# Optimization experiments

Hardware: AMD Instinct MI355X
Metric: run time of the kernel (lower is better)

Reference implementation:

```python
import jax, jax.numpy as jnp
import numpy as np

B, T, N, M, D = 4, 64, 32, 32, 128  # batch, time, price points, liquidity points, feature dim


def setup_inputs() -> dict:
    key = jax.random.key(0)
    ks = jax.random.split(key, 6)
    w = lambda k, shape: jax.random.normal(k, shape, jnp.float32) * 0.05
    return {
        "price": jax.random.normal(ks[0], (B, T, N, D), jnp.float32),
        "liquid": jax.random.normal(ks[1], (B, T, M, D), jnp.float32),
        "W_p": w(ks[2], (D, D)), "b_p": jnp.zeros((D,), jnp.float32),
        "W_v": w(ks[3], (D, D)), "b_v": jnp.zeros((D,), jnp.float32),
        "W1": w(ks[4], (4 * D, D)), "b1": jnp.zeros((D,), jnp.float32),
        "W2": w(ks[5], (D, D)), "b2": jnp.zeros((D,), jnp.float32),
    }


def reference(price, liquid, W_p, b_p, W_v, b_v, W1, b1, W2, b2):
    # proj_p / proj_v
    p = price @ W_p + b_p    # [B, T, N, D]
    v = liquid @ W_v + b_v   # [B, T, M, D]
    p4 = p[:, :, :, None, :]  # [B, T, N, 1, D]
    v4 = v[:, :, None, :, :]  # [B, T, 1, M, D]
    prod = p4 * v4            # [B, T, N, M, D]
    absdiff = jnp.abs(p4 - v4)
    full = (p.shape[0], p.shape[1], p.shape[2], v.shape[2], p.shape[3])
    pair = jnp.concatenate(
        [jnp.broadcast_to(p4, full), jnp.broadcast_to(v4, full), prod, absdiff],
        axis=-1,
    )  # [B, T, N, M, 4D]
    h = jax.nn.silu(pair @ W1 + b1)  # [B, T, N, M, D]
    grid = h @ W2 + b2               # [B, T, N, M, D]
    return grid.reshape(grid.shape[0], grid.shape[1], grid.shape[2] * grid.shape[3], grid.shape[4])
```

## Files before the change

kernel.cpp:

```cpp
#include <hip/hip_runtime.h>


typedef short  short8  __attribute__((ext_vector_type(8)));
typedef float  f32x4   __attribute__((ext_vector_type(4)));
typedef float  f32x16  __attribute__((ext_vector_type(16)));

#define DEV static __device__ __forceinline__

DEV float bf2f(unsigned short h) {
  unsigned u = ((unsigned)h) << 16;
  float f;
  __builtin_memcpy(&f, &u, 4);
  return f;
}
DEV unsigned short f2bf(float f) {
  unsigned u;
  __builtin_memcpy(&u, &f, 4);
  unsigned r = (u + 0x7FFFu + ((u >> 16) & 1u)) >> 16;
  return (unsigned short)r;
}

__global__ void k0_prep(const float* __restrict__ Wp, const float* __restrict__ bp,
                        const float* __restrict__ Wv, const float* __restrict__ bv,
                        const float* __restrict__ W1, const float* __restrict__ b1,
                        const float* __restrict__ W2,
                        unsigned short* __restrict__ w1cd, unsigned short* __restrict__ w2sw,
                        unsigned short* __restrict__ wpsw, unsigned short* __restrict__ gpsw,
                        unsigned short* __restrict__ wvsw, unsigned short* __restrict__ gvsw,
                        float* __restrict__ c1) {
  int t = blockIdx.x * 256 + threadIdx.x;
  if (t < 32768) {
    int j = t & 7, lane = (t >> 3) & 63, r2 = t >> 9;
    int ct = r2 & 3, kt = r2 >> 2;
    int k = kt * 16 + (lane >> 5) * 8 + j;
    int c = ct * 32 + (lane & 31);
    w1cd[t] = f2bf(W1[(256 + k) * 128 + c]);
  } else if (t < 114688) {
    int e = t - 32768;
    int sec = e >> 14;
    int f = e & 16383;
    int j = f & 7, lane = (f >> 3) & 63, r2 = f >> 9;
    if (sec == 0) {
      int ct = r2 & 3, kt = r2 >> 2;
      int k = kt * 16 + (lane >> 5) * 8 + j;
      int c = ct * 32 + (lane & 31);
      w2sw[f] = f2bf(W2[k * 128 + c]);
    } else {
      int kt = r2 & 3, ct = r2 >> 2;
      int k = kt * 32 + ((lane >> 4) & 3) * 8 + j;
      int n = ct * 16 + (lane & 15);
      if (sec == 1) {
        wpsw[f] = f2bf(Wp[k * 128 + n]);
      } else if (sec == 2) {
        float s = 0.f;
        for (int e2 = 0; e2 < 128; e2++) s += Wp[k * 128 + e2] * W1[e2 * 128 + n];
        gpsw[f] = f2bf(s);
      } else if (sec == 3) {
        wvsw[f] = f2bf(Wv[k * 128 + n]);
      } else {
        float s = 0.f;
        for (int e2 = 0; e2 < 128; e2++) s += Wv[k * 128 + e2] * W1[(128 + e2) * 128 + n];
        gvsw[f] = f2bf(s);
      }
    }
  } else if (t < 114816) {
    int c = t - 114688;
    float s = b1[c];
    for (int e2 = 0; e2 < 128; e2++)
      s += bp[e2] * W1[e2 * 128 + c] + bv[e2] * W1[(128 + e2) * 128 + c];
    c1[c] = s;
  }
}

__global__ __launch_bounds__(256, 2) void k1_proj(
    const float* __restrict__ price, const float* __restrict__ liquid,
    const float* __restrict__ bp, const float* __restrict__ bv, const float* __restrict__ c1,
    const unsigned short* __restrict__ wpsw, const unsigned short* __restrict__ gpsw,
    const unsigned short* __restrict__ wvsw, const unsigned short* __restrict__ gvsw,
    unsigned short* __restrict__ pbf, unsigned short* __restrict__ vbf,
    float* __restrict__ pAc, unsigned short* __restrict__ vbsw) {
  __shared__ __align__(16) unsigned short sA[128 * 136];
  int b = blockIdx.x;
  int chunk = b >> 2, sel = b & 3;
  int side = sel >> 1, half = sel & 1;
  int rowbase = chunk * 128;
  const float* src = side ? liquid : price;
  const unsigned short* bsw = side ? (half ? gvsw : wvsw) : (half ? gpsw : wpsw);
  int tid = threadIdx.x;

#pragma unroll
  for (int i = 0; i < 16; i++) {
    int e4 = i * 256 + tid;
    int row = e4 >> 5, c4 = (e4 & 31) * 4;
    float4 f = *(const float4*)(src + (rowbase + row) * 128 + c4);
    unsigned u0 = (unsigned)f2bf(f.x) | ((unsigned)f2bf(f.y) << 16);
    unsigned u1 = (unsigned)f2bf(f.z) | ((unsigned)f2bf(f.w) << 16);
    uint2 pk; pk.x = u0; pk.y = u1;
    *(uint2*)&sA[row * 136 + c4] = pk;
  }
  __syncthreads();

  int lane = tid & 63, w = tid >> 6;
  int l15 = lane & 15, q4 = lane >> 4;
  f32x4 acc[2][8] = {};
#pragma unroll
  for (int kt = 0; kt < 4; kt++) {
    short8 a0 = *(const short8*)&sA[(w * 32 + l15) * 136 + kt * 32 + q4 * 8];
    short8 a1 = *(const short8*)&sA[(w * 32 + 16 + l15) * 136 + kt * 32 + q4 * 8];
#pragma unroll
    for (int ct = 0; ct < 8; ct++) {
      short8 bfr = *(const short8*)(bsw + ((ct * 4 + kt) * 64 + lane) * 8);
      acc[0][ct] = __builtin_amdgcn_mfma_f32_16x16x32_bf16(a0, bfr, acc[0][ct], 0, 0, 0);
      acc[1][ct] = __builtin_amdgcn_mfma_f32_16x16x32_bf16(a1, bfr, acc[1][ct], 0, 0, 0);
    }
  }

#pragma unroll
  for (int rg = 0; rg < 2; rg++) {
#pragma unroll
    for (int ct = 0; ct < 8; ct++) {
      int col = ct * 16 + l15;
      int lrow0 = w * 32 + rg * 16 + q4 * 4;
#pragma unroll
      for (int ri = 0; ri < 4; ri++) {
        int grow = rowbase + lrow0 + ri;
        float val = acc[rg][ct][ri];
        if (side == 0) {
          if (half == 0) pbf[grow * 128 + col] = f2bf(val + bp[col]);
          else           pAc[grow * 128 + col] = val + c1[col];
        } else {
          if (half == 0) vbf[grow * 128 + col] = f2bf(val + bv[col]);
          else {
            int btl = grow >> 5, m = grow & 31;
            int idx = btl * 4096 +
                      ((((m >> 4) * 4 + (col >> 5)) * 64) + ((m >> 3) & 1) * 32 + (col & 31)) * 8 +
                      (m & 7);
            vbsw[idx] = f2bf(val);
          }
        }
      }
    }
  }
}

__global__ __launch_bounds__(256, 2) void k2_fused(
    const unsigned short* __restrict__ pbf, const unsigned short* __restrict__ vbf,
    const float* __restrict__ pAc, const unsigned short* __restrict__ w1cd,
    const unsigned short* __restrict__ vbsw, const unsigned short* __restrict__ w2sw,
    const float* __restrict__ b2, float* __restrict__ out) {
  __shared__ __align__(16) unsigned short sVf[4096];
  __shared__ __align__(16) unsigned short sP[8 * 136];
  __shared__ __align__(16) unsigned short sHt[4][32 * 136];
  int bt = blockIdx.x >> 2, n0 = (blockIdx.x & 3) * 8;
  int tid = threadIdx.x;

  if (tid < 128) {
    int row = tid >> 4, seg = tid & 15;
    *(uint4*)&sP[row * 136 + seg * 8] = *(const uint4*)(pbf + (bt * 32 + n0 + row) * 128 + seg * 8);
  }
#pragma unroll
  for (int g2 = 0; g2 < 2; g2++) {
    int g = tid * 2 + g2;
    int m = g & 31, k0 = (g >> 5) * 8;
    *(uint4*)&sVf[g * 8] = *(const uint4*)(vbf + (bt * 32 + m) * 128 + k0);
  }
  __syncthreads();

  int lane = tid & 63, w = tid >> 6;
  int m31 = lane & 31, hi = lane >> 5;
  int na = 2 * w, nb = 2 * w + 1;
  const unsigned short* vbswt = vbsw + bt * 4096;

  float pa0[4], pa1[4], bia[4];
#pragma unroll
  for (int ct = 0; ct < 4; ct++) {
    pa0[ct] = pAc[(bt * 32 + n0 + na) * 128 + ct * 32 + m31];
    pa1[ct] = pAc[(bt * 32 + n0 + nb) * 128 + ct * 32 + m31];
    bia[ct] = b2[ct * 32 + m31];
  }

  f32x16 acc0[4] = {};
  f32x16 acc1[4] = {};

#pragma unroll
  for (int kt = 0; kt < 8; kt++) {
    short8 vf = *(const short8*)&sVf[((kt * 2 + hi) * 32 + m31) * 8];
    short8 p0 = *(const short8*)&sP[na * 136 + kt * 16 + hi * 8];
    short8 p1 = *(const short8*)&sP[nb * 136 + kt * 16 + hi * 8];
    short8 x0, y0, x1, y1;
#pragma unroll
    for (int j = 0; j < 8; j++) {
      float vv = bf2f((unsigned short)vf[j]);
      float a = bf2f((unsigned short)p0[j]);
      float c = bf2f((unsigned short)p1[j]);
      x0[j] = (short)f2bf(a * vv);
      y0[j] = (short)f2bf(fabsf(a - vv));
      x1[j] = (short)f2bf(c * vv);
      y1[j] = (short)f2bf(fabsf(c - vv));
    }
    const unsigned short* bxb = w1cd + (kt * 4) * 512;
    const unsigned short* byb = w1cd + ((kt + 8) * 4) * 512;
#pragma unroll
    for (int ct = 0; ct < 4; ct++) {
      short8 bx = *(const short8*)(bxb + ct * 512 + lane * 8);
      short8 by = *(const short8*)(byb + ct * 512 + lane * 8);
      acc0[ct] = __builtin_amdgcn_mfma_f32_32x32x16_bf16(x0, bx, acc0[ct], 0, 0, 0);
      acc1[ct] = __builtin_amdgcn_mfma_f32_32x32x16_bf16(x1, bx, acc1[ct], 0, 0, 0);
      acc0[ct] = __builtin_amdgcn_mfma_f32_32x32x16_bf16(y0, by, acc0[ct], 0, 0, 0);
      acc1[ct] = __builtin_amdgcn_mfma_f32_32x32x16_bf16(y1, by, acc1[ct], 0, 0, 0);
    }
  }

#pragma unroll
  for (int kt2 = 0; kt2 < 2; kt2++) {
    short8 indf;
#pragma unroll
    for (int j = 0; j < 8; j++)
      indf[j] = (short)(((kt2 * 16 + hi * 8 + j) == m31) ? 0x3F80 : 0);
#pragma unroll
    for (int ct = 0; ct < 4; ct++) {
      short8 bi = *(const short8*)(vbswt + (kt2 * 4 + ct) * 512 + lane * 8);
      acc0[ct] = __builtin_amdgcn_mfma_f32_32x32x16_bf16(indf, bi, acc0[ct], 0, 0, 0);
      acc1[ct] = __builtin_amdgcn_mfma_f32_32x32x16_bf16(indf, bi, acc1[ct], 0, 0, 0);
    }
  }

#pragma unroll
  for (int ct = 0; ct < 4; ct++) {
#pragma unroll
    for (int i = 0; i < 16; i++) { acc0[ct][i] += pa0[ct]; acc1[ct][i] += pa1[ct]; }
  }

  unsigned short* sh = &sHt[w][0];
  auto tail = [&](const f32x16* A, int n) {
#pragma unroll
    for (int ct = 0; ct < 4; ct++) {
#pragma unroll
      for (int reg = 0; reg < 16; reg++) {
        float z = A[ct][reg];
        float hv = z / (1.f + __expf(-z));
        int mr = (reg & 3) + 8 * (reg >> 2) + 4 * hi;
        sh[mr * 136 + ct * 32 + m31] = f2bf(hv);
      }
    }
    short8 hf[8];
#pragma unroll
    for (int kt = 0; kt < 8; kt++)
      hf[kt] = *(const short8*)&sh[m31 * 136 + kt * 16 + hi * 8];
    f32x16 o[4] = {};
#pragma unroll
    for (int kt = 0; kt < 8; kt++) {
#pragma unroll
      for (int ct = 0; ct < 4; ct++) {
        short8 wf = *(const short8*)(w2sw + ((kt * 4 + ct) * 64 + lane) * 8);
        o[ct] = __builtin_amdgcn_mfma_f32_32x32x16_bf16(hf[kt], wf, o[ct], 0, 0, 0);
      }
    }
    int rowb = bt * 1024 + n * 32;
#pragma unroll
    for (int ct = 0; ct < 4; ct++) {
#pragma unroll
      for (int reg = 0; reg < 16; reg++) {
        int mr = (reg & 3) + 8 * (reg >> 2) + 4 * hi;
        out[(rowb + mr) * 128 + ct * 32 + m31] = o[ct][reg] + bia[ct];
      }
    }
  };
  tail(acc0, n0 + na);
  tail(acc1, n0 + nb);
}

extern "C" void kernel_launch(void* const* d_in, const int* in_sizes, int n_in,
                              void* d_out, int out_size, void* d_ws, size_t ws_size,
                              hipStream_t stream) {
  const float* price  = (const float*)d_in[0];
  const float* liquid = (const float*)d_in[1];
  const float* Wp     = (const float*)d_in[2];
  const float* bp     = (const float*)d_in[3];
  const float* Wv     = (const float*)d_in[4];
  const float* bv     = (const float*)d_in[5];
  const float* W1     = (const float*)d_in[6];
  const float* b1     = (const float*)d_in[7];
  const float* W2     = (const float*)d_in[8];
  const float* b2     = (const float*)d_in[9];

  char* ws = (char*)d_ws;
  unsigned short* w1cd = (unsigned short*)(ws + 0);
  unsigned short* w2sw = (unsigned short*)(ws + 65536);
  unsigned short* wpsw = (unsigned short*)(ws + 98304);
  unsigned short* gpsw = (unsigned short*)(ws + 131072);
  unsigned short* wvsw = (unsigned short*)(ws + 163840);
  unsigned short* gvsw = (unsigned short*)(ws + 196608);
  float*          c1   = (float*)(ws + 229376);
  unsigned short* pbf  = (unsigned short*)(ws + 262144);
  unsigned short* vbf  = (unsigned short*)(ws + 2359296);
  float*          pAc  = (float*)(ws + 4456448);
  unsigned short* vbsw = (unsigned short*)(ws + 8650752);

  hipLaunchKernelGGL(k0_prep, dim3(449), dim3(256), 0, stream,
                     Wp, bp, Wv, bv, W1, b1, W2, w1cd, w2sw, wpsw, gpsw, wvsw, gvsw, c1);
  hipLaunchKernelGGL(k1_proj, dim3(256), dim3(256), 0, stream,
                     price, liquid, bp, bv, c1, wpsw, gpsw, wvsw, gvsw, pbf, vbf, pAc, vbsw);
  hipLaunchKernelGGL(k2_fused, dim3(1024), dim3(256), 0, stream,
                     pbf, vbf, pAc, w1cd, vbsw, w2sw, b2, (float*)d_out);
}
```

Before: 242.8 us.

## Use truncating bf16 packing, fast reciprocal SiLU, and halve tail LDS staging

Replaces round-to-nearest bf16 conversion with byte-permute truncation (pk2) in the projection and pair-feature paths, and truncates h to bf16 with a shift. SiLU now uses a hardware reciprocal instead of a division. The second-GEMM tail is split into two halves of the hidden dimension, so each wave's LDS staging buffer shrinks to 32x72, which cuts shared memory and could raise occupancy. Truncation instead of rounding adds bias and slightly lowers accuracy.

```diff
diff --git a/kernel.cpp b/kernel.cpp
--- a/kernel.cpp
+++ b/kernel.cpp
@@ -19,6 +19,13 @@
   unsigned r = (u + 0x7FFFu + ((u >> 16) & 1u)) >> 16;
   return (unsigned short)r;
 }
+DEV unsigned pk2(float fh, float fl) {
+  return __builtin_amdgcn_perm(__float_as_uint(fh), __float_as_uint(fl), 0x07060302u);
+}
+DEV float lo16(unsigned u) { return __uint_as_float(u << 16); }
+DEV float hi16(unsigned u) { return __uint_as_float(u & 0xFFFF0000u); }
+
+union V8 { uint4 u; unsigned a[4]; short8 s; };
 
 __global__ void k0_prep(const float* __restrict__ Wp, const float* __restrict__ bp,
                         const float* __restrict__ Wv, const float* __restrict__ bv,
@@ -93,9 +100,9 @@
     int e4 = i * 256 + tid;
     int row = e4 >> 5, c4 = (e4 & 31) * 4;
     float4 f = *(const float4*)(src + (rowbase + row) * 128 + c4);
-    unsigned u0 = (unsigned)f2bf(f.x) | ((unsigned)f2bf(f.y) << 16);
-    unsigned u1 = (unsigned)f2bf(f.z) | ((unsigned)f2bf(f.w) << 16);
-    uint2 pk; pk.x = u0; pk.y = u1;
+    uint2 pk;
+    pk.x = pk2(f.y, f.x);
+    pk.y = pk2(f.w, f.z);
     *(uint2*)&sA[row * 136 + c4] = pk;
   }
   __syncthreads();
@@ -150,7 +157,7 @@
     const float* __restrict__ b2, float* __restrict__ out) {
   __shared__ __align__(16) unsigned short sVf[4096];
   __shared__ __align__(16) unsigned short sP[8 * 136];
-  __shared__ __align__(16) unsigned short sHt[4][32 * 136];
+  __shared__ __align__(16) unsigned short sHt[4][32 * 72];
   int bt = blockIdx.x >> 2, n0 = (blockIdx.x & 3) * 8;
   int tid = threadIdx.x;
 
@@ -184,19 +191,19 @@
 
 #pragma unroll
   for (int kt = 0; kt < 8; kt++) {
-    short8 vf = *(const short8*)&sVf[((kt * 2 + hi) * 32 + m31) * 8];
-    short8 p0 = *(const short8*)&sP[na * 136 + kt * 16 + hi * 8];
-    short8 p1 = *(const short8*)&sP[nb * 136 + kt * 16 + hi * 8];
-    short8 x0, y0, x1, y1;
-#pragma unroll
-    for (int j = 0; j < 8; j++) {
-      float vv = bf2f((unsigned short)vf[j]);
-      float a = bf2f((unsigned short)p0[j]);
-      float c = bf2f((unsigned short)p1[j]);
-      x0[j] = (short)f2bf(a * vv);
-      y0[j] = (short)f2bf(fabsf(a - vv));
-      x1[j] = (short)f2bf(c * vv);
-      y1[j] = (short)f2bf(fabsf(c - vv));
+    V8 vf, p0, p1, x0, y0, x1, y1;
+    vf.u = *(const uint4*)&sVf[((kt * 2 + hi) * 32 + m31) * 8];
+    p0.u = *(const uint4*)&sP[na * 136 + kt * 16 + hi * 8];
+    p1.u = *(const uint4*)&sP[nb * 136 + kt * 16 + hi * 8];
+#pragma unroll
+    for (int i = 0; i < 4; i++) {
+      float vl = lo16(vf.a[i]), vh = hi16(vf.a[i]);
+      float al = lo16(p0.a[i]), ah = hi16(p0.a[i]);
+      float cl = lo16(p1.a[i]), ch = hi16(p1.a[i]);
+      x0.a[i] = pk2(ah * vh, al * vl);
+      y0.a[i] = pk2(fabsf(ah - vh), fabsf(al - vl));
+      x1.a[i] = pk2(ch * vh, cl * vl);
+      y1.a[i] = pk2(fabsf(ch - vh), fabsf(cl - vl));
     }
     const unsigned short* bxb = w1cd + (kt * 4) * 512;
     const unsigned short* byb = w1cd + ((kt + 8) * 4) * 512;
@@ -204,10 +211,10 @@
     for (int ct = 0; ct < 4; ct++) {
       short8 bx = *(const short8*)(bxb + ct * 512 + lane * 8);
       short8 by = *(const short8*)(byb + ct * 512 + lane * 8);
-      acc0[ct] = __builtin_amdgcn_mfma_f32_32x32x16_bf16(x0, bx, acc0[ct], 0, 0, 0);
-      acc1[ct] = __builtin_amdgcn_mfma_f32_32x32x16_bf16(x1, bx, acc1[ct], 0, 0, 0);
-      acc0[ct] = __builtin_amdgcn_mfma_f32_32x32x16_bf16(y0, by, acc0[ct], 0, 0, 0);
-      acc1[ct] = __builtin_amdgcn_mfma_f32_32x32x16_bf16(y1, by, acc1[ct], 0, 0, 0);
+      acc0[ct] = __builtin_amdgcn_mfma_f32_32x32x16_bf16(x0.s, bx, acc0[ct], 0, 0, 0);
+      acc1[ct] = __builtin_amdgcn_mfma_f32_32x32x16_bf16(x1.s, bx, acc1[ct], 0, 0, 0);
+      acc0[ct] = __builtin_amdgcn_mfma_f32_32x32x16_bf16(y0.s, by, acc0[ct], 0, 0, 0);
+      acc1[ct] = __builtin_amdgcn_mfma_f32_32x32x16_bf16(y1.s, by, acc1[ct], 0, 0, 0);
     }
   }
 
@@ -233,27 +240,29 @@
 
   unsigned short* sh = &sHt[w][0];
   auto tail = [&](const f32x16* A, int n) {
-#pragma unroll
-    for (int ct = 0; ct < 4; ct++) {
-#pragma unroll
-      for (int reg = 0; reg < 16; reg++) {
-        float z = A[ct][reg];
-        float hv = z / (1.f + __expf(-z));
-        int mr = (reg & 3) + 8 * (reg >> 2) + 4 * hi;
-        sh[mr * 136 + ct * 32 + m31] = f2bf(hv);
-      }
-    }
-    short8 hf[8];
-#pragma unroll
-    for (int kt = 0; kt < 8; kt++)
-      hf[kt] = *(const short8*)&sh[m31 * 136 + kt * 16 + hi * 8];
     f32x16 o[4] = {};
 #pragma unroll
-    for (int kt = 0; kt < 8; kt++) {
-#pragma unroll
-      for (int ct = 0; ct < 4; ct++) {
-        short8 wf = *(const short8*)(w2sw + ((kt * 4 + ct) * 64 + lane) * 8);
-        o[ct] = __builtin_amdgcn_mfma_f32_32x32x16_bf16(hf[kt], wf, o[ct], 0, 0, 0);
+    for (int p = 0; p < 2; p++) {
+#pragma unroll
+      for (int c2 = 0; c2 < 2; c2++) {
+        int ct = p * 2 + c2;
+#pragma unroll
+        for (int reg = 0; reg < 16; reg++) {
+          float z = A[ct][reg];
+          float hv = z * __builtin_amdgcn_rcpf(1.f + __expf(-z));
+          int mr = (reg & 3) + 8 * (reg >> 2) + 4 * hi;
+          sh[mr * 72 + c2 * 32 + m31] = (unsigned short)(__float_as_uint(hv) >> 16);
+        }
+      }
+#pragma unroll
+      for (int kt = 0; kt < 4; kt++) {
+        int ktg = p * 4 + kt;
+        short8 hf = *(const short8*)&sh[m31 * 72 + kt * 16 + hi * 8];
+#pragma unroll
+        for (int ct = 0; ct < 4; ct++) {
+          short8 wf = *(const short8*)(w2sw + ((ktg * 4 + ct) * 64 + lane) * 8);
+          o[ct] = __builtin_amdgcn_mfma_f32_32x32x16_bf16(hf, wf, o[ct], 0, 0, 0);
+        }
       }
     }
     int rowb = bt * 1024 + n * 32;
```

New measurement: 242.7 us. About the same (-0.0%).
